# Kernel tuning notes

Hardware: AMD Instinct MI355X
Metric: run time of the kernel (lower is better)

The kernel has to match this reference:

```python
import jax, jax.numpy as jnp
import numpy as np

NUM_CLASSES = 2
NORM_EPS = 1e-12   # F.normalize default
COS_EPS = 1e-8     # nn.CosineSimilarity default
MEAN_EPS = 1e-6


def _l2_normalize_c(x):
    # normalize over channel dim (dim=1), per (batch, pixel) -- matches
    # F.normalize(x.view(-1,16,256*256), dim=1)
    n = jnp.sqrt(jnp.sum(x * x, axis=1, keepdims=True))
    return x / jnp.maximum(n, NORM_EPS)


def _cos_c(a, b):
    # cosine similarity along channel dim, torch semantics
    dot = jnp.sum(a * b, axis=1)
    na = jnp.sqrt(jnp.sum(a * a, axis=1))
    nb = jnp.sqrt(jnp.sum(b * b, axis=1))
    return dot / jnp.maximum(na * nb, COS_EPS)


def setup_inputs() -> dict:
    key = jax.random.key(0)
    k1, k2, k3 = jax.random.split(key, 3)
    preds_S = jax.random.normal(k1, (32, 16, 256, 256), dtype=jnp.float32)
    preds_T = jax.random.normal(k2, (32, 16, 256, 256), dtype=jnp.float32)
    target = jax.random.randint(k3, (32, 256, 256), 0, NUM_CLASSES, dtype=jnp.int64)
    return {"preds_S": preds_S, "preds_T": preds_T, "target": target}


def reference(preds_S, preds_T, target):
    feat_S = _l2_normalize_c(preds_S)  # [B,16,H,W]
    feat_T = _l2_normalize_c(preds_T)
    # target is already HxW == feature size, so nearest upsample is identity
    tar = target[:, None, :, :].astype(feat_S.dtype)  # [B,1,H,W], broadcasts over C

    center_S, center_T = feat_S, feat_T
    center_S_FS, center_T_FS = feat_S, feat_T
    for i in range(NUM_CLASSES):
        mask = (tar == i).astype(feat_S.dtype)  # [B,1,H,W]
        cnt = jnp.sum(mask, axis=(-2, -1)) + MEAN_EPS  # [B,1]
        mean_S = (jnp.sum(mask * feat_S, axis=(-2, -1)) / cnt)[:, :, None, None]  # [B,16,1,1]
        mean_T = (jnp.sum(mask * feat_T, axis=(-2, -1)) / cnt)[:, :, None, None]
        center_S = (1.0 - mask) * center_S + mask * mean_S
        center_T = (1.0 - mask) * center_T + mask * mean_T
        center_S_FS = mask * center_S_FS + (1.0 - mask) * mean_S
        center_T_FS = mask * center_T_FS + (1.0 - mask) * mean_T

    pcsim_S = jnp.exp(_cos_c(feat_S, center_S) - _cos_c(feat_S, center_S_FS))
    pcsim_T = jnp.exp(_cos_c(feat_T, center_T) - _cos_c(feat_T, center_T_FS))
    return jnp.mean((pcsim_S - pcsim_T) ** 2)
```

## Files before the change

### kernel.cpp

```cpp
#include <hip/hip_runtime.h>
#include <math.h>

#define NBATCH 32
#define NCH 16
#define HW 65536
#define SLICES1 64
#define SLICES2 64
#define TPB 256

#define WS_SUMS_S 0
#define WS_SUMS_T 1024
#define WS_N1     2048
#define WS_LOSS   2080
#define WS_FLOATS 2112

__device__ __forceinline__ float wave_sum(float v) {
#pragma unroll
  for (int off = 32; off > 0; off >>= 1) v += __shfl_down(v, off, 64);
  return v;
}

__global__ __launch_bounds__(TPB) void k_sums(const float* __restrict__ S,
                                              const float* __restrict__ T,
                                              const int* __restrict__ tgt,
                                              float* __restrict__ ws) {
  const int b = blockIdx.y;
  const int slice = blockIdx.x;
  const int which = blockIdx.z;
  const int tid = threadIdx.x;
  const int lane = tid & 63, wid = tid >> 6;

  const float* Xb = (which ? T : S) + (size_t)b * NCH * HW;
  const int* tb = tgt + (size_t)b * HW;
  float* dst = ws + (which ? WS_SUMS_T : WS_SUMS_S) + b * 32;

  const int p = slice * (HW / SLICES1) + tid * 4;

  const int4 tv = *(const int4*)(tb + p);
  float4 x[NCH];
#pragma unroll
  for (int c = 0; c < NCH; ++c) x[c] = *(const float4*)(Xb + (size_t)c * HW + p);

  const float m0 = (tv.x == 1) ? 1.f : 0.f;
  const float m1 = (tv.y == 1) ? 1.f : 0.f;
  const float m2 = (tv.z == 1) ? 1.f : 0.f;
  const float m3 = (tv.w == 1) ? 1.f : 0.f;

  float s0a = 0.f, s0b = 0.f, s1a = 0.f, s1b = 0.f;
  float s2a = 0.f, s2b = 0.f, s3a = 0.f, s3b = 0.f;
#pragma unroll
  for (int c = 0; c < NCH; c += 2) {
    s0a = fmaf(x[c].x, x[c].x, s0a);   s0b = fmaf(x[c + 1].x, x[c + 1].x, s0b);
    s1a = fmaf(x[c].y, x[c].y, s1a);   s1b = fmaf(x[c + 1].y, x[c + 1].y, s1b);
    s2a = fmaf(x[c].z, x[c].z, s2a);   s2b = fmaf(x[c + 1].z, x[c + 1].z, s2b);
    s3a = fmaf(x[c].w, x[c].w, s3a);   s3b = fmaf(x[c + 1].w, x[c + 1].w, s3b);
  }
  const float i0 = 1.f / fmaxf(sqrtf(s0a + s0b), 1e-12f);
  const float i1 = 1.f / fmaxf(sqrtf(s1a + s1b), 1e-12f);
  const float i2 = 1.f / fmaxf(sqrtf(s2a + s2b), 1e-12f);
  const float i3 = 1.f / fmaxf(sqrtf(s3a + s3b), 1e-12f);

  float c0s[NCH], c1s[NCH];
#pragma unroll
  for (int c = 0; c < NCH; ++c) {
    const float f0 = x[c].x * i0, f1 = x[c].y * i1;
    const float f2 = x[c].z * i2, f3 = x[c].w * i3;
    const float t_ = (f0 + f1) + (f2 + f3);
    const float m_ = fmaf(f0, m0, fmaf(f1, m1, fmaf(f2, m2, f3 * m3)));
    c1s[c] = m_;
    c0s[c] = t_ - m_;
  }
  float n1 = (m0 + m1) + (m2 + m3);

#pragma unroll
  for (int c = 0; c < NCH; ++c) { c0s[c] = wave_sum(c0s[c]); c1s[c] = wave_sum(c1s[c]); }
  n1 = wave_sum(n1);

  __shared__ float red[4][36];
  if (lane == 0) {
#pragma unroll
    for (int c = 0; c < NCH; ++c) { red[wid][c] = c0s[c]; red[wid][16 + c] = c1s[c]; }
    red[wid][32] = n1;
  }
  __syncthreads();
  if (tid < 33) {
    const float v = red[0][tid] + red[1][tid] + red[2][tid] + red[3][tid];
    if (tid < 32) atomicAdd(dst + tid, v);
    else if (which == 0) atomicAdd(ws + WS_N1 + b, v);
  }
}

__device__ __forceinline__ float pc_one(float ss, float d0, float d1, int t,
                                        float nm0, float nm1) {
  const float n = sqrtf(ss);
  const float inv = 1.f / fmaxf(n, 1e-12f);
  const float na = n * inv;
  const float c0 = (d0 * inv) / fmaxf(na * nm0, 1e-8f);
  const float c1 = (d1 * inv) / fmaxf(na * nm1, 1e-8f);
  return expf((t == 1) ? (c1 - c0) : (c0 - c1));
}

__global__ __launch_bounds__(TPB) void k_pass2(const float* __restrict__ S,
                                               const float* __restrict__ T,
                                               const int* __restrict__ tgt,
                                               float* __restrict__ ws) {
  __shared__ float sm[68];
  __shared__ float red[4];
  const int b = blockIdx.y;
  const int slice = blockIdx.x;
  const int tid = threadIdx.x;

  if (tid < 64) {
    const int t = tid >> 5, cls = (tid >> 4) & 1, ch = tid & 15;
    const float n1v = ws[WS_N1 + b];
    const float cnt = (cls ? n1v : ((float)HW - n1v)) + 1e-6f;
    const float s = ws[(t ? WS_SUMS_T : WS_SUMS_S) + b * 32 + cls * 16 + ch];
    sm[tid] = s / cnt;
  }
  __syncthreads();
  if (tid < 4) {
    float ss = 0.f;
    const int base_ = (tid >> 1) * 32 + (tid & 1) * 16;
#pragma unroll
    for (int c = 0; c < NCH; ++c) { const float v = sm[base_ + c]; ss = fmaf(v, v, ss); }
    sm[64 + tid] = sqrtf(ss);
  }
  __syncthreads();

  const int p = slice * (HW / SLICES2) + tid * 4;
  const float* Sb = S + (size_t)b * NCH * HW;
  const float* Tb = T + (size_t)b * NCH * HW;
  const int4 tv = *(const int4*)(tgt + (size_t)b * HW + p);

  float4 xS[NCH], xT[NCH];
#pragma unroll
  for (int c = 0; c < NCH; ++c) xS[c] = *(const float4*)(Sb + (size_t)c * HW + p);
#pragma unroll
  for (int c = 0; c < NCH; ++c) xT[c] = *(const float4*)(Tb + (size_t)c * HW + p);

  const float nmS0 = sm[64], nmS1 = sm[65], nmT0 = sm[66], nmT1 = sm[67];

  float4 ssv = {0, 0, 0, 0}, d0 = {0, 0, 0, 0}, d1 = {0, 0, 0, 0};
#pragma unroll
  for (int c = 0; c < NCH; ++c) {
    const float4 x = xS[c];
    const float w0 = sm[c], w1 = sm[16 + c];
    ssv.x = fmaf(x.x, x.x, ssv.x); ssv.y = fmaf(x.y, x.y, ssv.y);
    ssv.z = fmaf(x.z, x.z, ssv.z); ssv.w = fmaf(x.w, x.w, ssv.w);
    d0.x = fmaf(x.x, w0, d0.x); d0.y = fmaf(x.y, w0, d0.y);
    d0.z = fmaf(x.z, w0, d0.z); d0.w = fmaf(x.w, w0, d0.w);
    d1.x = fmaf(x.x, w1, d1.x); d1.y = fmaf(x.y, w1, d1.y);
    d1.z = fmaf(x.z, w1, d1.z); d1.w = fmaf(x.w, w1, d1.w);
  }
  const float pcS0 = pc_one(ssv.x, d0.x, d1.x, tv.x, nmS0, nmS1);
  const float pcS1 = pc_one(ssv.y, d0.y, d1.y, tv.y, nmS0, nmS1);
  const float pcS2 = pc_one(ssv.z, d0.z, d1.z, tv.z, nmS0, nmS1);
  const float pcS3 = pc_one(ssv.w, d0.w, d1.w, tv.w, nmS0, nmS1);

  ssv = {0, 0, 0, 0}; d0 = {0, 0, 0, 0}; d1 = {0, 0, 0, 0};
#pragma unroll
  for (int c = 0; c < NCH; ++c) {
    const float4 x = xT[c];
    const float w0 = sm[32 + c], w1 = sm[48 + c];
    ssv.x = fmaf(x.x, x.x, ssv.x); ssv.y = fmaf(x.y, x.y, ssv.y);
    ssv.z = fmaf(x.z, x.z, ssv.z); ssv.w = fmaf(x.w, x.w, ssv.w);
    d0.x = fmaf(x.x, w0, d0.x); d0.y = fmaf(x.y, w0, d0.y);
    d0.z = fmaf(x.z, w0, d0.z); d0.w = fmaf(x.w, w0, d0.w);
    d1.x = fmaf(x.x, w1, d1.x); d1.y = fmaf(x.y, w1, d1.y);
    d1.z = fmaf(x.z, w1, d1.z); d1.w = fmaf(x.w, w1, d1.w);
  }
  const float pcT0 = pc_one(ssv.x, d0.x, d1.x, tv.x, nmT0, nmT1);
  const float pcT1 = pc_one(ssv.y, d0.y, d1.y, tv.y, nmT0, nmT1);
  const float pcT2 = pc_one(ssv.z, d0.z, d1.z, tv.z, nmT0, nmT1);
  const float pcT3 = pc_one(ssv.w, d0.w, d1.w, tv.w, nmT0, nmT1);

  const float e0 = pcS0 - pcT0, e1 = pcS1 - pcT1;
  const float e2 = pcS2 - pcT2, e3 = pcS3 - pcT3;
  float lacc = e0 * e0 + e1 * e1 + e2 * e2 + e3 * e3;

  lacc = wave_sum(lacc);
  if ((tid & 63) == 0) red[tid >> 6] = lacc;
  __syncthreads();
  if (tid == 0)
    atomicAdd(ws + WS_LOSS + b, red[0] + red[1] + red[2] + red[3]);
}

__global__ void k_final(const float* __restrict__ ws, float* __restrict__ out) {
  float s = 0.f;
  for (int b = 0; b < NBATCH; ++b) s += ws[WS_LOSS + b];
  out[0] = s * (1.f / 2097152.f);
}

extern "C" void kernel_launch(void* const* d_in, const int* in_sizes, int n_in,
                              void* d_out, int out_size, void* d_ws, size_t ws_size,
                              hipStream_t stream) {
  const float* S = (const float*)d_in[0];
  const float* T = (const float*)d_in[1];
  const int* tgt = (const int*)d_in[2];
  float* ws = (float*)d_ws;
  float* out = (float*)d_out;

  hipMemsetAsync(d_ws, 0, WS_FLOATS * sizeof(float), stream);
  dim3 g1(SLICES1, NBATCH, 2);
  k_sums<<<g1, TPB, 0, stream>>>(S, T, tgt, ws);
  dim3 g2(SLICES2, NBATCH);
  k_pass2<<<g2, TPB, 0, stream>>>(S, T, tgt, ws);
  k_final<<<1, 1, 0, stream>>>(ws, out);
}
```

Baseline: 330.5 us.

## Software-pipeline both passes with double-buffered multi-iteration loops per block

Each block now covers several pixel chunks instead of one. k_sums loops over 8 chunks of 2 pixels per thread with A/B register buffers, and k_pass2 loops over 4 chunks with S/T loads interleaved against compute. The intent is to overlap global loads with math, cut the number of atomics and block-launch overhead, and start pass2 loads before its shared-memory setup and barrier. k_final now uses a wave reduction. The risk is lower occupancy from the large register buffers, even with the launch_bounds hints, and fewer blocks in the grid.

```diff
diff --git a/kernel.cpp b/kernel.cpp
--- a/kernel.cpp
+++ b/kernel.cpp
@@ -4,8 +4,8 @@
 #define NBATCH 32
 #define NCH 16
 #define HW 65536
-#define SLICES1 64
-#define SLICES2 64
+#define SLICES1 16
+#define SLICES2 16
 #define TPB 256
 
 #define WS_SUMS_S 0
@@ -20,10 +20,10 @@
   return v;
 }
 
-__global__ __launch_bounds__(TPB) void k_sums(const float* __restrict__ S,
-                                              const float* __restrict__ T,
-                                              const int* __restrict__ tgt,
-                                              float* __restrict__ ws) {
+__global__ __launch_bounds__(TPB, 3) void k_sums(const float* __restrict__ S,
+                                                 const float* __restrict__ T,
+                                                 const int* __restrict__ tgt,
+                                                 float* __restrict__ ws) {
   const int b = blockIdx.y;
   const int slice = blockIdx.x;
   const int which = blockIdx.z;
@@ -34,43 +34,60 @@
   const int* tb = tgt + (size_t)b * HW;
   float* dst = ws + (which ? WS_SUMS_T : WS_SUMS_S) + b * 32;
 
-  const int p = slice * (HW / SLICES1) + tid * 4;
-
-  const int4 tv = *(const int4*)(tb + p);
-  float4 x[NCH];
-#pragma unroll
-  for (int c = 0; c < NCH; ++c) x[c] = *(const float4*)(Xb + (size_t)c * HW + p);
-
-  const float m0 = (tv.x == 1) ? 1.f : 0.f;
-  const float m1 = (tv.y == 1) ? 1.f : 0.f;
-  const float m2 = (tv.z == 1) ? 1.f : 0.f;
-  const float m3 = (tv.w == 1) ? 1.f : 0.f;
-
-  float s0a = 0.f, s0b = 0.f, s1a = 0.f, s1b = 0.f;
-  float s2a = 0.f, s2b = 0.f, s3a = 0.f, s3b = 0.f;
-#pragma unroll
-  for (int c = 0; c < NCH; c += 2) {
-    s0a = fmaf(x[c].x, x[c].x, s0a);   s0b = fmaf(x[c + 1].x, x[c + 1].x, s0b);
-    s1a = fmaf(x[c].y, x[c].y, s1a);   s1b = fmaf(x[c + 1].y, x[c + 1].y, s1b);
-    s2a = fmaf(x[c].z, x[c].z, s2a);   s2b = fmaf(x[c + 1].z, x[c + 1].z, s2b);
-    s3a = fmaf(x[c].w, x[c].w, s3a);   s3b = fmaf(x[c + 1].w, x[c + 1].w, s3b);
-  }
-  const float i0 = 1.f / fmaxf(sqrtf(s0a + s0b), 1e-12f);
-  const float i1 = 1.f / fmaxf(sqrtf(s1a + s1b), 1e-12f);
-  const float i2 = 1.f / fmaxf(sqrtf(s2a + s2b), 1e-12f);
-  const float i3 = 1.f / fmaxf(sqrtf(s3a + s3b), 1e-12f);
+  const int base = slice * (HW / SLICES1) + tid * 2;
 
   float c0s[NCH], c1s[NCH];
 #pragma unroll
-  for (int c = 0; c < NCH; ++c) {
-    const float f0 = x[c].x * i0, f1 = x[c].y * i1;
-    const float f2 = x[c].z * i2, f3 = x[c].w * i3;
-    const float t_ = (f0 + f1) + (f2 + f3);
-    const float m_ = fmaf(f0, m0, fmaf(f1, m1, fmaf(f2, m2, f3 * m3)));
-    c1s[c] = m_;
-    c0s[c] = t_ - m_;
-  }
-  float n1 = (m0 + m1) + (m2 + m3);
+  for (int c = 0; c < NCH; ++c) { c0s[c] = 0.f; c1s[c] = 0.f; }
+  float n1 = 0.f;
+
+  float2 bufA[NCH], bufB[NCH];
+  int2 tvA, tvB;
+
+#define KS_LOAD(BUF, TV, IT) do { \
+    const int p_ = base + (IT) * (TPB * 2); \
+    TV = *(const int2*)(tb + p_); \
+    _Pragma("unroll") \
+    for (int c = 0; c < NCH; ++c) BUF[c] = *(const float2*)(Xb + (size_t)c * HW + p_); \
+  } while (0)
+
+#define KS_COMP(BUF, TV) do { \
+    const float m0 = (TV.x == 1) ? 1.f : 0.f; \
+    const float m1 = (TV.y == 1) ? 1.f : 0.f; \
+    n1 += m0 + m1; \
+    float s0a = 0.f, s0b = 0.f, s1a = 0.f, s1b = 0.f; \
+    _Pragma("unroll") \
+    for (int c = 0; c < NCH; c += 2) { \
+      s0a = fmaf(BUF[c].x, BUF[c].x, s0a); \
+      s1a = fmaf(BUF[c].y, BUF[c].y, s1a); \
+      s0b = fmaf(BUF[c + 1].x, BUF[c + 1].x, s0b); \
+      s1b = fmaf(BUF[c + 1].y, BUF[c + 1].y, s1b); \
+    } \
+    const float i0 = 1.f / fmaxf(sqrtf(s0a + s0b), 1e-12f); \
+    const float i1 = 1.f / fmaxf(sqrtf(s1a + s1b), 1e-12f); \
+    _Pragma("unroll") \
+    for (int c = 0; c < NCH; ++c) { \
+      const float f0 = BUF[c].x * i0, f1 = BUF[c].y * i1; \
+      const float t_ = f0 + f1; \
+      const float m_ = fmaf(f0, m0, f1 * m1); \
+      c1s[c] += m_; \
+      c0s[c] += t_ - m_; \
+    } \
+  } while (0)
+
+  KS_LOAD(bufA, tvA, 0);
+  KS_LOAD(bufB, tvB, 1);
+  KS_COMP(bufA, tvA);  KS_LOAD(bufA, tvA, 2);
+  KS_COMP(bufB, tvB);  KS_LOAD(bufB, tvB, 3);
+  KS_COMP(bufA, tvA);  KS_LOAD(bufA, tvA, 4);
+  KS_COMP(bufB, tvB);  KS_LOAD(bufB, tvB, 5);
+  KS_COMP(bufA, tvA);  KS_LOAD(bufA, tvA, 6);
+  KS_COMP(bufB, tvB);  KS_LOAD(bufB, tvB, 7);
+  KS_COMP(bufA, tvA);
+  KS_COMP(bufB, tvB);
+
+#undef KS_LOAD
+#undef KS_COMP
 
 #pragma unroll
   for (int c = 0; c < NCH; ++c) { c0s[c] = wave_sum(c0s[c]); c1s[c] = wave_sum(c1s[c]); }
@@ -100,15 +117,37 @@
   return expf((t == 1) ? (c1 - c0) : (c0 - c1));
 }
 
-__global__ __launch_bounds__(TPB) void k_pass2(const float* __restrict__ S,
-                                               const float* __restrict__ T,
-                                               const int* __restrict__ tgt,
-                                               float* __restrict__ ws) {
-  __shared__ float sm[68];
+__global__ __launch_bounds__(TPB, 2) void k_pass2(const float* __restrict__ S,
+                                                  const float* __restrict__ T,
+                                                  const int* __restrict__ tgt,
+                                                  float* __restrict__ ws) {
+  __shared__ __align__(16) float sm[72];
   __shared__ float red[4];
   const int b = blockIdx.y;
   const int slice = blockIdx.x;
   const int tid = threadIdx.x;
+
+  const int base = slice * (HW / SLICES2) + tid * 4;
+  const float* Sb = S + (size_t)b * NCH * HW;
+  const float* Tb = T + (size_t)b * NCH * HW;
+  const int* tb = tgt + (size_t)b * HW;
+
+  float4 Sx[NCH], Tx[NCH];
+  int4 tvA, tvB;
+
+#define P2_LTV(TV, IT) TV = *(const int4*)(tb + base + (IT) * (TPB * 4))
+#define P2_LS(IT) do { const int p_ = base + (IT) * (TPB * 4); \
+    _Pragma("unroll") \
+    for (int c = 0; c < NCH; ++c) Sx[c] = *(const float4*)(Sb + (size_t)c * HW + p_); \
+  } while (0)
+#define P2_LT(IT) do { const int p_ = base + (IT) * (TPB * 4); \
+    _Pragma("unroll") \
+    for (int c = 0; c < NCH; ++c) Tx[c] = *(const float4*)(Tb + (size_t)c * HW + p_); \
+  } while (0)
+
+  P2_LTV(tvA, 0);
+  P2_LS(0);
+  P2_LT(0);
 
   if (tid < 64) {
     const int t = tid >> 5, cls = (tid >> 4) & 1, ch = tid & 15;
@@ -127,56 +166,67 @@
   }
   __syncthreads();
 
-  const int p = slice * (HW / SLICES2) + tid * 4;
-  const float* Sb = S + (size_t)b * NCH * HW;
-  const float* Tb = T + (size_t)b * NCH * HW;
-  const int4 tv = *(const int4*)(tgt + (size_t)b * HW + p);
-
-  float4 xS[NCH], xT[NCH];
-#pragma unroll
-  for (int c = 0; c < NCH; ++c) xS[c] = *(const float4*)(Sb + (size_t)c * HW + p);
-#pragma unroll
-  for (int c = 0; c < NCH; ++c) xT[c] = *(const float4*)(Tb + (size_t)c * HW + p);
-
+  const float4* smq = (const float4*)sm;
   const float nmS0 = sm[64], nmS1 = sm[65], nmT0 = sm[66], nmT1 = sm[67];
 
-  float4 ssv = {0, 0, 0, 0}, d0 = {0, 0, 0, 0}, d1 = {0, 0, 0, 0};
-#pragma unroll
-  for (int c = 0; c < NCH; ++c) {
-    const float4 x = xS[c];
-    const float w0 = sm[c], w1 = sm[16 + c];
-    ssv.x = fmaf(x.x, x.x, ssv.x); ssv.y = fmaf(x.y, x.y, ssv.y);
-    ssv.z = fmaf(x.z, x.z, ssv.z); ssv.w = fmaf(x.w, x.w, ssv.w);
-    d0.x = fmaf(x.x, w0, d0.x); d0.y = fmaf(x.y, w0, d0.y);
-    d0.z = fmaf(x.z, w0, d0.z); d0.w = fmaf(x.w, w0, d0.w);
-    d1.x = fmaf(x.x, w1, d1.x); d1.y = fmaf(x.y, w1, d1.y);
-    d1.z = fmaf(x.z, w1, d1.z); d1.w = fmaf(x.w, w1, d1.w);
-  }
-  const float pcS0 = pc_one(ssv.x, d0.x, d1.x, tv.x, nmS0, nmS1);
-  const float pcS1 = pc_one(ssv.y, d0.y, d1.y, tv.y, nmS0, nmS1);
-  const float pcS2 = pc_one(ssv.z, d0.z, d1.z, tv.z, nmS0, nmS1);
-  const float pcS3 = pc_one(ssv.w, d0.w, d1.w, tv.w, nmS0, nmS1);
-
-  ssv = {0, 0, 0, 0}; d0 = {0, 0, 0, 0}; d1 = {0, 0, 0, 0};
-#pragma unroll
-  for (int c = 0; c < NCH; ++c) {
-    const float4 x = xT[c];
-    const float w0 = sm[32 + c], w1 = sm[48 + c];
-    ssv.x = fmaf(x.x, x.x, ssv.x); ssv.y = fmaf(x.y, x.y, ssv.y);
-    ssv.z = fmaf(x.z, x.z, ssv.z); ssv.w = fmaf(x.w, x.w, ssv.w);
-    d0.x = fmaf(x.x, w0, d0.x); d0.y = fmaf(x.y, w0, d0.y);
-    d0.z = fmaf(x.z, w0, d0.z); d0.w = fmaf(x.w, w0, d0.w);
-    d1.x = fmaf(x.x, w1, d1.x); d1.y = fmaf(x.y, w1, d1.y);
-    d1.z = fmaf(x.z, w1, d1.z); d1.w = fmaf(x.w, w1, d1.w);
-  }
-  const float pcT0 = pc_one(ssv.x, d0.x, d1.x, tv.x, nmT0, nmT1);
-  const float pcT1 = pc_one(ssv.y, d0.y, d1.y, tv.y, nmT0, nmT1);
-  const float pcT2 = pc_one(ssv.z, d0.z, d1.z, tv.z, nmT0, nmT1);
-  const float pcT3 = pc_one(ssv.w, d0.w, d1.w, tv.w, nmT0, nmT1);
-
-  const float e0 = pcS0 - pcT0, e1 = pcS1 - pcT1;
-  const float e2 = pcS2 - pcT2, e3 = pcS3 - pcT3;
-  float lacc = e0 * e0 + e1 * e1 + e2 * e2 + e3 * e3;
+  float lacc = 0.f;
+  float pcS0, pcS1, pcS2, pcS3;
+
+#define P2_ACC(X, W0, W1) do { \
+    ssv.x = fmaf(X.x, X.x, ssv.x); ssv.y = fmaf(X.y, X.y, ssv.y); \
+    ssv.z = fmaf(X.z, X.z, ssv.z); ssv.w = fmaf(X.w, X.w, ssv.w); \
+    d0.x = fmaf(X.x, W0, d0.x); d0.y = fmaf(X.y, W0, d0.y); \
+    d0.z = fmaf(X.z, W0, d0.z); d0.w = fmaf(X.w, W0, d0.w); \
+    d1.x = fmaf(X.x, W1, d1.x); d1.y = fmaf(X.y, W1, d1.y); \
+    d1.z = fmaf(X.z, W1, d1.z); d1.w = fmaf(X.w, W1, d1.w); \
+  } while (0)
+
+#define P2_COMPS(TV) do { \
+    float4 ssv = {0, 0, 0, 0}, d0 = {0, 0, 0, 0}, d1 = {0, 0, 0, 0}; \
+    _Pragma("unroll") \
+    for (int c4 = 0; c4 < 4; ++c4) { \
+      const float4 w0 = smq[c4], w1 = smq[4 + c4]; \
+      P2_ACC(Sx[4 * c4 + 0], w0.x, w1.x); P2_ACC(Sx[4 * c4 + 1], w0.y, w1.y); \
+      P2_ACC(Sx[4 * c4 + 2], w0.z, w1.z); P2_ACC(Sx[4 * c4 + 3], w0.w, w1.w); \
+    } \
+    pcS0 = pc_one(ssv.x, d0.x, d1.x, TV.x, nmS0, nmS1); \
+    pcS1 = pc_one(ssv.y, d0.y, d1.y, TV.y, nmS0, nmS1); \
+    pcS2 = pc_one(ssv.z, d0.z, d1.z, TV.z, nmS0, nmS1); \
+    pcS3 = pc_one(ssv.w, d0.w, d1.w, TV.w, nmS0, nmS1); \
+  } while (0)
+
+#define P2_COMPT(TV) do { \
+    float4 ssv = {0, 0, 0, 0}, d0 = {0, 0, 0, 0}, d1 = {0, 0, 0, 0}; \
+    _Pragma("unroll") \
+    for (int c4 = 0; c4 < 4; ++c4) { \
+      const float4 w0 = smq[8 + c4], w1 = smq[12 + c4]; \
+      P2_ACC(Tx[4 * c4 + 0], w0.x, w1.x); P2_ACC(Tx[4 * c4 + 1], w0.y, w1.y); \
+      P2_ACC(Tx[4 * c4 + 2], w0.z, w1.z); P2_ACC(Tx[4 * c4 + 3], w0.w, w1.w); \
+    } \
+    const float pcT0 = pc_one(ssv.x, d0.x, d1.x, TV.x, nmT0, nmT1); \
+    const float pcT1 = pc_one(ssv.y, d0.y, d1.y, TV.y, nmT0, nmT1); \
+    const float pcT2 = pc_one(ssv.z, d0.z, d1.z, TV.z, nmT0, nmT1); \
+    const float pcT3 = pc_one(ssv.w, d0.w, d1.w, TV.w, nmT0, nmT1); \
+    const float e0 = pcS0 - pcT0, e1 = pcS1 - pcT1; \
+    const float e2 = pcS2 - pcT2, e3 = pcS3 - pcT3; \
+    lacc += e0 * e0 + e1 * e1 + e2 * e2 + e3 * e3; \
+  } while (0)
+
+  P2_COMPS(tvA);  P2_LS(1);  P2_LTV(tvB, 1);
+  P2_COMPT(tvA);  P2_LT(1);
+  P2_COMPS(tvB);  P2_LS(2);  P2_LTV(tvA, 2);
+  P2_COMPT(tvB);  P2_LT(2);
+  P2_COMPS(tvA);  P2_LS(3);  P2_LTV(tvB, 3);
+  P2_COMPT(tvA);  P2_LT(3);
+  P2_COMPS(tvB);
+  P2_COMPT(tvB);
+
+#undef P2_LTV
+#undef P2_LS
+#undef P2_LT
+#undef P2_ACC
+#undef P2_COMPS
+#undef P2_COMPT
 
   lacc = wave_sum(lacc);
   if ((tid & 63) == 0) red[tid >> 6] = lacc;
@@ -186,9 +236,10 @@
 }
 
 __global__ void k_final(const float* __restrict__ ws, float* __restrict__ out) {
-  float s = 0.f;
-  for (int b = 0; b < NBATCH; ++b) s += ws[WS_LOSS + b];
-  out[0] = s * (1.f / 2097152.f);
+  const int lane = threadIdx.x & 63;
+  float v = (lane < NBATCH) ? ws[WS_LOSS + lane] : 0.f;
+  v = wave_sum(v);
+  if (lane == 0) out[0] = v * (1.f / 2097152.f);
 }
 
 extern "C" void kernel_launch(void* const* d_in, const int* in_sizes, int n_in,
@@ -205,5 +256,5 @@
   k_sums<<<g1, TPB, 0, stream>>>(S, T, tgt, ws);
   dim3 g2(SLICES2, NBATCH);
   k_pass2<<<g2, TPB, 0, stream>>>(S, T, tgt, ws);
-  k_final<<<1, 1, 0, stream>>>(ws, out);
-}
+  k_final<<<1, 64, 0, stream>>>(ws, out);
+}
```

Measured after the change: 441.1 us. +33.5%, slower.

## Stagger channel loads, loop over pixels per block, and use LDS reduction

Applied to the files above, without the earlier changes.

Both passes now process more pixels per block via an inner loop and halve the grid. Channel reads are rotated by a per-wave/block offset to spread concurrent DRAM accesses. The first pass replaces per-channel wave shuffles with an LDS transpose reduction. The second pass uses float2 loads to cut register pressure and raise occupancy. The final reduction uses one wave. Narrower loads and fewer blocks may lower achieved bandwidth.

```diff
diff --git a/kernel.cpp b/kernel.cpp
--- a/kernel.cpp
+++ b/kernel.cpp
@@ -4,8 +4,8 @@
 #define NBATCH 32
 #define NCH 16
 #define HW 65536
-#define SLICES1 64
-#define SLICES2 64
+#define SLICES1 32
+#define SLICES2 32
 #define TPB 256
 
 #define WS_SUMS_S 0
@@ -28,66 +28,87 @@
   const int slice = blockIdx.x;
   const int which = blockIdx.z;
   const int tid = threadIdx.x;
-  const int lane = tid & 63, wid = tid >> 6;
+  const int wid = tid >> 6;
 
   const float* Xb = (which ? T : S) + (size_t)b * NCH * HW;
   const int* tb = tgt + (size_t)b * HW;
   float* dst = ws + (which ? WS_SUMS_T : WS_SUMS_S) + b * 32;
 
-  const int p = slice * (HW / SLICES1) + tid * 4;
-
-  const int4 tv = *(const int4*)(tb + p);
-  float4 x[NCH];
-#pragma unroll
-  for (int c = 0; c < NCH; ++c) x[c] = *(const float4*)(Xb + (size_t)c * HW + p);
-
-  const float m0 = (tv.x == 1) ? 1.f : 0.f;
-  const float m1 = (tv.y == 1) ? 1.f : 0.f;
-  const float m2 = (tv.z == 1) ? 1.f : 0.f;
-  const float m3 = (tv.w == 1) ? 1.f : 0.f;
-
-  float s0a = 0.f, s0b = 0.f, s1a = 0.f, s1b = 0.f;
-  float s2a = 0.f, s2b = 0.f, s3a = 0.f, s3b = 0.f;
-#pragma unroll
-  for (int c = 0; c < NCH; c += 2) {
-    s0a = fmaf(x[c].x, x[c].x, s0a);   s0b = fmaf(x[c + 1].x, x[c + 1].x, s0b);
-    s1a = fmaf(x[c].y, x[c].y, s1a);   s1b = fmaf(x[c + 1].y, x[c + 1].y, s1b);
-    s2a = fmaf(x[c].z, x[c].z, s2a);   s2b = fmaf(x[c + 1].z, x[c + 1].z, s2b);
-    s3a = fmaf(x[c].w, x[c].w, s3a);   s3b = fmaf(x[c + 1].w, x[c + 1].w, s3b);
-  }
-  const float i0 = 1.f / fmaxf(sqrtf(s0a + s0b), 1e-12f);
-  const float i1 = 1.f / fmaxf(sqrtf(s1a + s1b), 1e-12f);
-  const float i2 = 1.f / fmaxf(sqrtf(s2a + s2b), 1e-12f);
-  const float i3 = 1.f / fmaxf(sqrtf(s3a + s3b), 1e-12f);
-
-  float c0s[NCH], c1s[NCH];
-#pragma unroll
-  for (int c = 0; c < NCH; ++c) {
-    const float f0 = x[c].x * i0, f1 = x[c].y * i1;
-    const float f2 = x[c].z * i2, f3 = x[c].w * i3;
-    const float t_ = (f0 + f1) + (f2 + f3);
-    const float m_ = fmaf(f0, m0, fmaf(f1, m1, fmaf(f2, m2, f3 * m3)));
-    c1s[c] = m_;
-    c0s[c] = t_ - m_;
-  }
-  float n1 = (m0 + m1) + (m2 + m3);
-
-#pragma unroll
-  for (int c = 0; c < NCH; ++c) { c0s[c] = wave_sum(c0s[c]); c1s[c] = wave_sum(c1s[c]); }
+  const int off = (wid + ((slice & 3) << 2) + b + (which << 3)) & 15;
+
+  const int base = slice * (HW / SLICES1) + tid * 4;
+
+  float acc0[NCH], acc1[NCH];
+#pragma unroll
+  for (int i = 0; i < NCH; ++i) { acc0[i] = 0.f; acc1[i] = 0.f; }
+  float n1 = 0.f;
+
+  for (int it = 0; it < 2; ++it) {
+    const int p = base + it * (TPB * 4);
+    const int4 tv = *(const int4*)(tb + p);
+    float4 x[NCH];
+#pragma unroll
+    for (int i = 0; i < NCH; ++i) {
+      const int cc = (i + off) & 15;
+      x[i] = *(const float4*)(Xb + (size_t)cc * HW + p);
+    }
+
+    const float m0 = (tv.x == 1) ? 1.f : 0.f;
+    const float m1 = (tv.y == 1) ? 1.f : 0.f;
+    const float m2 = (tv.z == 1) ? 1.f : 0.f;
+    const float m3 = (tv.w == 1) ? 1.f : 0.f;
+    n1 += (m0 + m1) + (m2 + m3);
+
+    float s0a = 0.f, s0b = 0.f, s1a = 0.f, s1b = 0.f;
+    float s2a = 0.f, s2b = 0.f, s3a = 0.f, s3b = 0.f;
+#pragma unroll
+    for (int i = 0; i < NCH; i += 2) {
+      s0a = fmaf(x[i].x, x[i].x, s0a);   s0b = fmaf(x[i + 1].x, x[i + 1].x, s0b);
+      s1a = fmaf(x[i].y, x[i].y, s1a);   s1b = fmaf(x[i + 1].y, x[i + 1].y, s1b);
+      s2a = fmaf(x[i].z, x[i].z, s2a);   s2b = fmaf(x[i + 1].z, x[i + 1].z, s2b);
+      s3a = fmaf(x[i].w, x[i].w, s3a);   s3b = fmaf(x[i + 1].w, x[i + 1].w, s3b);
+    }
+    const float i0 = 1.f / fmaxf(sqrtf(s0a + s0b), 1e-12f);
+    const float i1 = 1.f / fmaxf(sqrtf(s1a + s1b), 1e-12f);
+    const float i2 = 1.f / fmaxf(sqrtf(s2a + s2b), 1e-12f);
+    const float i3 = 1.f / fmaxf(sqrtf(s3a + s3b), 1e-12f);
+
+#pragma unroll
+    for (int i = 0; i < NCH; ++i) {
+      const float f0 = x[i].x * i0, f1 = x[i].y * i1;
+      const float f2 = x[i].z * i2, f3 = x[i].w * i3;
+      const float t_ = (f0 + f1) + (f2 + f3);
+      const float m_ = fmaf(f0, m0, fmaf(f1, m1, fmaf(f2, m2, f3 * m3)));
+      acc1[i] += m_;
+      acc0[i] += t_ - m_;
+    }
+  }
+
+  __shared__ float lds[32][TPB + 1];
+  __shared__ float redn[4];
+#pragma unroll
+  for (int i = 0; i < NCH; ++i) {
+    const int r = (i + off) & 15;
+    lds[r][tid] = acc0[i];
+    lds[16 + r][tid] = acc1[i];
+  }
   n1 = wave_sum(n1);
-
-  __shared__ float red[4][36];
-  if (lane == 0) {
-#pragma unroll
-    for (int c = 0; c < NCH; ++c) { red[wid][c] = c0s[c]; red[wid][16 + c] = c1s[c]; }
-    red[wid][32] = n1;
-  }
-  __syncthreads();
-  if (tid < 33) {
-    const float v = red[0][tid] + red[1][tid] + red[2][tid] + red[3][tid];
-    if (tid < 32) atomicAdd(dst + tid, v);
-    else if (which == 0) atomicAdd(ws + WS_N1 + b, v);
-  }
+  if ((tid & 63) == 0) redn[wid] = n1;
+  __syncthreads();
+
+  const int row = tid >> 3, seg = tid & 7;
+  float s = 0.f;
+#pragma unroll
+  for (int k0 = 0; k0 < 32; ++k0) {
+    const int k = (k0 + seg * 4) & 31;
+    s += lds[row][seg * 32 + k];
+  }
+  s += __shfl_down(s, 4, 8);
+  s += __shfl_down(s, 2, 8);
+  s += __shfl_down(s, 1, 8);
+  if (seg == 0) atomicAdd(dst + row, s);
+  if (tid == 0 && which == 0)
+    atomicAdd(ws + WS_N1 + b, redn[0] + redn[1] + redn[2] + redn[3]);
 }
 
 __device__ __forceinline__ float pc_one(float ss, float d0, float d1, int t,
@@ -104,11 +125,20 @@
                                                const float* __restrict__ T,
                                                const int* __restrict__ tgt,
                                                float* __restrict__ ws) {
-  __shared__ float sm[68];
+  __shared__ __align__(16) float sm[72];
   __shared__ float red[4];
   const int b = blockIdx.y;
   const int slice = blockIdx.x;
   const int tid = threadIdx.x;
+  const int wid = tid >> 6;
+
+  const int offS = (wid + ((slice & 3) << 2) + b) & 15;
+  const int offT = (offS + 8) & 15;
+
+  const int base = slice * (HW / SLICES2) + tid * 2;
+  const float* Sb = S + (size_t)b * NCH * HW;
+  const float* Tb = T + (size_t)b * NCH * HW;
+  const int* tb = tgt + (size_t)b * HW;
 
   if (tid < 64) {
     const int t = tid >> 5, cls = (tid >> 4) & 1, ch = tid & 15;
@@ -127,56 +157,47 @@
   }
   __syncthreads();
 
-  const int p = slice * (HW / SLICES2) + tid * 4;
-  const float* Sb = S + (size_t)b * NCH * HW;
-  const float* Tb = T + (size_t)b * NCH * HW;
-  const int4 tv = *(const int4*)(tgt + (size_t)b * HW + p);
-
-  float4 xS[NCH], xT[NCH];
-#pragma unroll
-  for (int c = 0; c < NCH; ++c) xS[c] = *(const float4*)(Sb + (size_t)c * HW + p);
-#pragma unroll
-  for (int c = 0; c < NCH; ++c) xT[c] = *(const float4*)(Tb + (size_t)c * HW + p);
-
   const float nmS0 = sm[64], nmS1 = sm[65], nmT0 = sm[66], nmT1 = sm[67];
-
-  float4 ssv = {0, 0, 0, 0}, d0 = {0, 0, 0, 0}, d1 = {0, 0, 0, 0};
-#pragma unroll
-  for (int c = 0; c < NCH; ++c) {
-    const float4 x = xS[c];
-    const float w0 = sm[c], w1 = sm[16 + c];
-    ssv.x = fmaf(x.x, x.x, ssv.x); ssv.y = fmaf(x.y, x.y, ssv.y);
-    ssv.z = fmaf(x.z, x.z, ssv.z); ssv.w = fmaf(x.w, x.w, ssv.w);
-    d0.x = fmaf(x.x, w0, d0.x); d0.y = fmaf(x.y, w0, d0.y);
-    d0.z = fmaf(x.z, w0, d0.z); d0.w = fmaf(x.w, w0, d0.w);
-    d1.x = fmaf(x.x, w1, d1.x); d1.y = fmaf(x.y, w1, d1.y);
-    d1.z = fmaf(x.z, w1, d1.z); d1.w = fmaf(x.w, w1, d1.w);
-  }
-  const float pcS0 = pc_one(ssv.x, d0.x, d1.x, tv.x, nmS0, nmS1);
-  const float pcS1 = pc_one(ssv.y, d0.y, d1.y, tv.y, nmS0, nmS1);
-  const float pcS2 = pc_one(ssv.z, d0.z, d1.z, tv.z, nmS0, nmS1);
-  const float pcS3 = pc_one(ssv.w, d0.w, d1.w, tv.w, nmS0, nmS1);
-
-  ssv = {0, 0, 0, 0}; d0 = {0, 0, 0, 0}; d1 = {0, 0, 0, 0};
-#pragma unroll
-  for (int c = 0; c < NCH; ++c) {
-    const float4 x = xT[c];
-    const float w0 = sm[32 + c], w1 = sm[48 + c];
-    ssv.x = fmaf(x.x, x.x, ssv.x); ssv.y = fmaf(x.y, x.y, ssv.y);
-    ssv.z = fmaf(x.z, x.z, ssv.z); ssv.w = fmaf(x.w, x.w, ssv.w);
-    d0.x = fmaf(x.x, w0, d0.x); d0.y = fmaf(x.y, w0, d0.y);
-    d0.z = fmaf(x.z, w0, d0.z); d0.w = fmaf(x.w, w0, d0.w);
-    d1.x = fmaf(x.x, w1, d1.x); d1.y = fmaf(x.y, w1, d1.y);
-    d1.z = fmaf(x.z, w1, d1.z); d1.w = fmaf(x.w, w1, d1.w);
-  }
-  const float pcT0 = pc_one(ssv.x, d0.x, d1.x, tv.x, nmT0, nmT1);
-  const float pcT1 = pc_one(ssv.y, d0.y, d1.y, tv.y, nmT0, nmT1);
-  const float pcT2 = pc_one(ssv.z, d0.z, d1.z, tv.z, nmT0, nmT1);
-  const float pcT3 = pc_one(ssv.w, d0.w, d1.w, tv.w, nmT0, nmT1);
-
-  const float e0 = pcS0 - pcT0, e1 = pcS1 - pcT1;
-  const float e2 = pcS2 - pcT2, e3 = pcS3 - pcT3;
-  float lacc = e0 * e0 + e1 * e1 + e2 * e2 + e3 * e3;
+  float lacc = 0.f;
+
+  for (int it = 0; it < 4; ++it) {
+    const int p = base + it * (TPB * 2);
+    const int2 tv = *(const int2*)(tb + p);
+    float2 xs[NCH], xt[NCH];
+#pragma unroll
+    for (int i = 0; i < NCH; ++i)
+      xs[i] = *(const float2*)(Sb + (size_t)((i + offS) & 15) * HW + p);
+#pragma unroll
+    for (int i = 0; i < NCH; ++i)
+      xt[i] = *(const float2*)(Tb + (size_t)((i + offT) & 15) * HW + p);
+
+    float ss0 = 0.f, ss1 = 0.f, d00 = 0.f, d01 = 0.f, d10 = 0.f, d11 = 0.f;
+#pragma unroll
+    for (int i = 0; i < NCH; ++i) {
+      const int cc = (i + offS) & 15;
+      const float w0 = sm[cc], w1 = sm[16 + cc];
+      ss0 = fmaf(xs[i].x, xs[i].x, ss0); ss1 = fmaf(xs[i].y, xs[i].y, ss1);
+      d00 = fmaf(xs[i].x, w0, d00);      d01 = fmaf(xs[i].y, w0, d01);
+      d10 = fmaf(xs[i].x, w1, d10);      d11 = fmaf(xs[i].y, w1, d11);
+    }
+    const float pcS0 = pc_one(ss0, d00, d10, tv.x, nmS0, nmS1);
+    const float pcS1 = pc_one(ss1, d01, d11, tv.y, nmS0, nmS1);
+
+    ss0 = 0.f; ss1 = 0.f; d00 = 0.f; d01 = 0.f; d10 = 0.f; d11 = 0.f;
+#pragma unroll
+    for (int i = 0; i < NCH; ++i) {
+      const int cc = (i + offT) & 15;
+      const float w0 = sm[32 + cc], w1 = sm[48 + cc];
+      ss0 = fmaf(xt[i].x, xt[i].x, ss0); ss1 = fmaf(xt[i].y, xt[i].y, ss1);
+      d00 = fmaf(xt[i].x, w0, d00);      d01 = fmaf(xt[i].y, w0, d01);
+      d10 = fmaf(xt[i].x, w1, d10);      d11 = fmaf(xt[i].y, w1, d11);
+    }
+    const float pcT0 = pc_one(ss0, d00, d10, tv.x, nmT0, nmT1);
+    const float pcT1 = pc_one(ss1, d01, d11, tv.y, nmT0, nmT1);
+
+    const float e0 = pcS0 - pcT0, e1 = pcS1 - pcT1;
+    lacc += e0 * e0 + e1 * e1;
+  }
 
   lacc = wave_sum(lacc);
   if ((tid & 63) == 0) red[tid >> 6] = lacc;
@@ -186,9 +207,10 @@
 }
 
 __global__ void k_final(const float* __restrict__ ws, float* __restrict__ out) {
-  float s = 0.f;
-  for (int b = 0; b < NBATCH; ++b) s += ws[WS_LOSS + b];
-  out[0] = s * (1.f / 2097152.f);
+  const int lane = threadIdx.x & 63;
+  float v = (lane < NBATCH) ? ws[WS_LOSS + lane] : 0.f;
+  v = wave_sum(v);
+  if (lane == 0) out[0] = v * (1.f / 2097152.f);
 }
 
 extern "C" void kernel_launch(void* const* d_in, const int* in_sizes, int n_in,
@@ -205,5 +227,5 @@
   k_sums<<<g1, TPB, 0, stream>>>(S, T, tgt, ws);
   dim3 g2(SLICES2, NBATCH);
   k_pass2<<<g2, TPB, 0, stream>>>(S, T, tgt, ws);
-  k_final<<<1, 1, 0, stream>>>(ws, out);
-}
+  k_final<<<1, 64, 0, stream>>>(ws, out);
+}
```

After: 335.1 us. Within noise of the previous version (+1.4%).
